# Performance work log

Measured on AMD Instinct MI355X. Metric: run time of the kernel, lower is better.

## Reference

```python
import jax, jax.numpy as jnp
import numpy as np

B, IN, H, OUT = 4096, 1024, 2048, 1024
EPS = 1e-5  # added to std (not variance), matching the torch module


def _ln(z, a, b):
    # torch.std default is unbiased (ddof=1); eps added to sigma
    mu = jnp.mean(z, axis=1, keepdims=True)
    sigma = jnp.std(z, axis=1, ddof=1, keepdims=True)
    return (z - mu) / (sigma + EPS) * a + b


def setup_inputs() -> dict:
    key = jax.random.key(0)
    ks = iter(jax.random.split(key, 40))
    W = lambda i, o: (jax.random.normal(next(ks), (o, i), jnp.float32) / np.sqrt(i)).astype(jnp.float32)
    bz = lambda o: jnp.zeros((o,), jnp.float32)
    d = {
        "inp": jax.random.normal(next(ks), (B, IN), jnp.float32),
        "h_0": jax.random.normal(next(ks), (B, H), jnp.float32),
        "c_0": jax.random.normal(next(ks), (B, H), jnp.float32),
        # h-side gate linears (H -> H)
        "Wfh": W(H, H), "bfh": bz(H), "Wih": W(H, H), "bih": bz(H),
        "Wch": W(H, H), "bch": bz(H), "Woh": W(H, H), "boh": bz(H),
        # x-side gate linears (IN -> H)
        "Wfx": W(IN, H), "bfx": bz(H), "Wix": W(IN, H), "bix": bz(H),
        "Wcx": W(IN, H), "bcx": bz(H), "Wox": W(IN, H), "box": bz(H),
        # decoder (H -> OUT)
        "Wdec": W(H, OUT), "bdec": bz(OUT),
        # LayerNormalization params (a2 ones, b2 zeros), shape (1, H)
        "ax": jnp.ones((1, H), jnp.float32), "bx": jnp.zeros((1, H), jnp.float32),
        "ah": jnp.ones((1, H), jnp.float32), "bh": jnp.zeros((1, H), jnp.float32),
        "ac": jnp.ones((1, H), jnp.float32), "bc": jnp.zeros((1, H), jnp.float32),
    }
    return d


def reference(inp, h_0, c_0,
              Wfh, bfh, Wih, bih, Wch, bch, Woh, boh,
              Wfx, bfx, Wix, bix, Wcx, bcx, Wox, box,
              Wdec, bdec, ax, bx, ah, bh, ac, bc):
    lin = lambda x, W, b: x @ W.T + b
    gate = lambda wx, bx_, wh, bh_: (_ln(lin(inp, wx, bx_), ax, bx)
                                     + _ln(lin(h_0, wh, bh_), ah, bh))
    f_g = jax.nn.sigmoid(gate(Wfx, bfx, Wfh, bfh))
    i_g = jax.nn.sigmoid(gate(Wix, bix, Wih, bih))
    c_tilda = jnp.tanh(gate(Wcx, bcx, Wch, bch))
    cx = f_g * c_0 + i_g * c_tilda
    o_g = jax.nn.sigmoid(gate(Wox, box, Woh, boh))
    hx = o_g * jnp.tanh(_ln(cx, ac, bc))
    out = lin(hx, Wdec, bdec)  # decoder applied to hidden state (vectorized over batch)
    return (out, hx, cx)
```

## Files before the change

kernel.cpp:

```cpp
#include <hip/hip_runtime.h>

#define NB   4096
#define NIN  1024
#define NH   2048
#define NOUT 1024
#define NH4  8192

typedef short short8 __attribute__((ext_vector_type(8)));
typedef float f32x4 __attribute__((ext_vector_type(4)));
typedef float f32x16 __attribute__((ext_vector_type(16)));
typedef unsigned short ushort8v __attribute__((ext_vector_type(8)));

__device__ __forceinline__ float bf2f(unsigned short u) {
  union { unsigned int i; float f; } c; c.i = ((unsigned int)u) << 16; return c.f;
}
__device__ __forceinline__ unsigned short f2bf(float f) {
  union { float f; unsigned int i; } c; c.f = f;
  unsigned int u = c.i;
  u += 0x7FFFu + ((u >> 16) & 1u);
  return (unsigned short)(u >> 16);
}
__device__ __forceinline__ float sigf(float x) { return 1.0f / (1.0f + __expf(-x)); }
__device__ __forceinline__ float tanh_f(float x) { return 1.0f - 2.0f / (__expf(2.0f * x) + 1.0f); }

#define CNT_INP  ((size_t)NB * NIN)
#define CNT_H0   ((size_t)NB * NH)
#define CNT_WXG  ((size_t)NH * NIN)
#define CNT_WHG  ((size_t)NH * NH)
#define CNT_WD   ((size_t)NOUT * NH)
#define OFF_XB   ((size_t)0)
#define OFF_H0B  (OFF_XB + CNT_INP)
#define OFF_HXB  (OFF_H0B + CNT_H0)
#define OFF_WX   (OFF_HXB + CNT_H0)
#define OFF_WH   (OFF_WX + 4 * CNT_WXG)
#define OFF_WD   (OFF_WH + 4 * CNT_WHG)
#define OFF_ZX   (OFF_WD + CNT_WD)
#define OFF_ZH   (OFF_ZX + (size_t)NB * NH4)
#define CVT_TOTAL (OFF_WD + CNT_WD)

struct CvtArgs { const float* src[11]; };

__global__ __launch_bounds__(256) void cvt_all(CvtArgs a, unsigned short* __restrict__ dstBase) {
  const size_t i = ((size_t)blockIdx.x * 256 + threadIdx.x) * 8;
  if (i >= CVT_TOTAL) return;
  const size_t cnt[11] = {CNT_INP, CNT_H0, CNT_WXG, CNT_WXG, CNT_WXG, CNT_WXG,
                          CNT_WHG, CNT_WHG, CNT_WHG, CNT_WHG, CNT_WD};
  const size_t dst[11] = {OFF_XB, OFF_H0B,
                          OFF_WX, OFF_WX + CNT_WXG, OFF_WX + 2 * CNT_WXG, OFF_WX + 3 * CNT_WXG,
                          OFF_WH, OFF_WH + CNT_WHG, OFF_WH + 2 * CNT_WHG, OFF_WH + 3 * CNT_WHG,
                          OFF_WD};
  size_t base = 0;
#pragma unroll
  for (int s = 0; s < 11; s++) {
    if (i < base + cnt[s]) {
      const size_t off = i - base;
      const float* sp = a.src[s] + off;
      float4 v0 = *(const float4*)(sp);
      float4 v1 = *(const float4*)(sp + 4);
      ushort8v o;
      o[0] = f2bf(v0.x); o[1] = f2bf(v0.y); o[2] = f2bf(v0.z); o[3] = f2bf(v0.w);
      o[4] = f2bf(v1.x); o[5] = f2bf(v1.y); o[6] = f2bf(v1.z); o[7] = f2bf(v1.w);
      *(ushort8v*)(dstBase + dst[s] + off) = o;
      return;
    }
    base += cnt[s];
  }
}

__device__ __forceinline__ void gload16(const void* g, void* l) {
  __builtin_amdgcn_global_load_lds((const __attribute__((address_space(1))) void*)g,
                                   (__attribute__((address_space(3))) void*)l, 16, 0, 0);
}

#define SCH0  __builtin_amdgcn_sched_barrier(0)
#define BARR  __builtin_amdgcn_s_barrier()
#define LGKM0 asm volatile("s_waitcnt lgkmcnt(0)" ::: "memory")
#define VMC6  asm volatile("s_waitcnt vmcnt(6)" ::: "memory")
#define VMC0  asm volatile("s_waitcnt vmcnt(0)" ::: "memory")
#define PRIO1 __builtin_amdgcn_s_setprio(1)
#define PRIO0 __builtin_amdgcn_s_setprio(0)
#define MFMA16(A, B, C) __builtin_amdgcn_mfma_f32_16x16x32_bf16((A), (B), (C), 0, 0, 0)

#define SWZ(R) (((R) & 7) ^ ((((R) >> 3) & 3) << 1))


__device__ __forceinline__ void stage_half(const unsigned short* __restrict__ G, size_t thrOff, int K,
                                           int R0, int H, int T, unsigned short* __restrict__ ldbase, int wid) {
  const unsigned short* gs = G + thrOff + (size_t)(R0 + H * 128) * K + (size_t)T * 64;
  unsigned short* ld = ldbase + (H * 128 + wid * 8) * 64;
  gload16(gs, ld);
  gload16(gs + (size_t)64 * K, ld + 4096);
}

__device__ __forceinline__ void tile_step(
    const unsigned short* __restrict__ sA, const unsigned short* __restrict__ sB,
    unsigned short* __restrict__ sAc, unsigned short* __restrict__ sBc, unsigned short* __restrict__ sAn,
    int t1, int t2,
    const unsigned short* __restrict__ Ag, const unsigned short* __restrict__ Bg,
    size_t thrOff, int m0, int n0, int K, int wid,
    const int (&oA)[8][2], const int (&oB)[4][2], f32x4 (&acc)[8][4]) {
  short8 b01[2][2], b23[2][2], alo[4][2], ahi[4][2];

#pragma unroll
  for (int n = 0; n < 2; n++) {
    b01[n][0] = *(const short8*)&sB[oB[n][0]];
    b01[n][1] = *(const short8*)&sB[oB[n][1]];
  }
#pragma unroll
  for (int m = 0; m < 2; m++) {
    alo[m][0] = *(const short8*)&sA[oA[m][0]];
    alo[m][1] = *(const short8*)&sA[oA[m][1]];
  }
  stage_half(Ag, thrOff, K, m0, 1, t1, sAn, wid);
  SCH0;
#pragma unroll
  for (int m = 2; m < 4; m++) {
    alo[m][0] = *(const short8*)&sA[oA[m][0]];
    alo[m][1] = *(const short8*)&sA[oA[m][1]];
  }
  SCH0;
  PRIO1;
#pragma unroll
  for (int m = 0; m < 2; m++)
#pragma unroll
    for (int n = 0; n < 2; n++) {
      acc[m][n] = MFMA16(alo[m][0], b01[n][0], acc[m][n]);
      acc[m][n] = MFMA16(alo[m][1], b01[n][1], acc[m][n]);
    }
  PRIO0; SCH0;
#pragma unroll
  for (int n = 0; n < 2; n++) {
    b23[n][0] = *(const short8*)&sB[oB[2 + n][0]];
    b23[n][1] = *(const short8*)&sB[oB[2 + n][1]];
  }
  SCH0;
  PRIO1;
#pragma unroll
  for (int m = 2; m < 4; m++)
#pragma unroll
    for (int n = 0; n < 2; n++) {
      acc[m][n] = MFMA16(alo[m][0], b01[n][0], acc[m][n]);
      acc[m][n] = MFMA16(alo[m][1], b01[n][1], acc[m][n]);
    }
  PRIO0; SCH0;
#pragma unroll
  for (int m = 0; m < 4; m++) {
    ahi[m][0] = *(const short8*)&sA[oA[4 + m][0]];
    ahi[m][1] = *(const short8*)&sA[oA[4 + m][1]];
  }
  SCH0;
  PRIO1;
#pragma unroll
  for (int m = 0; m < 4; m++)
#pragma unroll
    for (int n = 0; n < 2; n++) {
      acc[m][2 + n] = MFMA16(alo[m][0], b23[n][0], acc[m][2 + n]);
      acc[m][2 + n] = MFMA16(alo[m][1], b23[n][1], acc[m][2 + n]);
    }
  PRIO0;
  SCH0; BARR; SCH0;
  stage_half(Bg, thrOff, K, n0, 0, t2, sBc, wid);
  stage_half(Bg, thrOff, K, n0, 1, t2, sBc, wid);
  SCH0;
  PRIO1;
#pragma unroll
  for (int m = 0; m < 4; m++)
#pragma unroll
    for (int n = 0; n < 2; n++) {
      acc[4 + m][n] = MFMA16(ahi[m][0], b01[n][0], acc[4 + m][n]);
      acc[4 + m][n] = MFMA16(ahi[m][1], b01[n][1], acc[4 + m][n]);
    }
  PRIO0;
  SCH0; BARR; SCH0;
  stage_half(Ag, thrOff, K, m0, 0, t2, sAc, wid);
  SCH0;
  PRIO1;
#pragma unroll
  for (int m = 0; m < 4; m++)
#pragma unroll
    for (int n = 0; n < 2; n++) {
      acc[4 + m][2 + n] = MFMA16(ahi[m][0], b23[n][0], acc[4 + m][2 + n]);
      acc[4 + m][2 + n] = MFMA16(ahi[m][1], b23[n][1], acc[4 + m][2 + n]);
    }
  PRIO0;
  VMC6;
  SCH0; BARR; SCH0;
}

__global__ __launch_bounds__(512) void gemm_dual8(
    const unsigned short* __restrict__ Xb, const unsigned short* __restrict__ Wx,
    const unsigned short* __restrict__ H0b, const unsigned short* __restrict__ Wh,
    const float* bx0, const float* bx1, const float* bx2, const float* bx3,
    const float* bh0, const float* bh1, const float* bh2, const float* bh3,
    unsigned short* __restrict__ Zx, unsigned short* __restrict__ Zh) {
  __shared__ __align__(16) unsigned short As[2][256 * 64];
  __shared__ __align__(16) unsigned short Bs[2][256 * 64];

  const unsigned short* Ag; const unsigned short* Bg;
  const float *p0, *p1, *p2, *p3; unsigned short* Cg; int K;
  if (blockIdx.z == 0) { Ag = Xb;  Bg = Wx; Cg = Zx; K = NIN; p0 = bx0; p1 = bx1; p2 = bx2; p3 = bx3; }
  else                 { Ag = H0b; Bg = Wh; Cg = Zh; K = NH;  p0 = bh0; p1 = bh1; p2 = bh2; p3 = bh3; }

  const int t    = threadIdx.x;
  const int wid  = t >> 6;
  const int lane = t & 63;
  const int m15  = lane & 15;
  const int g4   = lane >> 4;
  const int wm   = wid >> 2;
  const int wn   = wid & 3;
  const int rloc = lane >> 3;
  const int slot = lane & 7;
  const int ck   = slot ^ rloc ^ ((wid & 3) << 1);
  const int m0   = blockIdx.y * 256;
  const int n0   = blockIdx.x * 256;
  const int NT   = K >> 6;
  const size_t thrOff = (size_t)(wid * 8 + rloc) * K + ck * 8;

  int oA[8][2], oB[4][2];
#pragma unroll
  for (int m = 0; m < 4; m++) {
    const int r1 = wm * 128 + m * 16 + m15;
    const int r2 = r1 + 64;
#pragma unroll
    for (int h = 0; h < 2; h++) {
      oA[m][h]     = r1 * 64 + (((h * 4 + g4) ^ SWZ(r1)) * 8);
      oA[4 + m][h] = r2 * 64 + (((h * 4 + g4) ^ SWZ(r2)) * 8);
    }
  }
#pragma unroll
  for (int n = 0; n < 4; n++) {
    const int r = wn * 64 + n * 16 + m15;
#pragma unroll
    for (int h = 0; h < 2; h++) oB[n][h] = r * 64 + (((h * 4 + g4) ^ SWZ(r)) * 8);
  }

  f32x4 acc[8][4];
#pragma unroll
  for (int m = 0; m < 8; m++)
#pragma unroll
    for (int n = 0; n < 4; n++)
#pragma unroll
      for (int r = 0; r < 4; r++) acc[m][n][r] = 0.f;

  stage_half(Ag, thrOff, K, m0, 0, 0, As[0], wid);
  stage_half(Ag, thrOff, K, m0, 1, 0, As[0], wid);
  stage_half(Bg, thrOff, K, n0, 0, 0, Bs[0], wid);
  stage_half(Bg, thrOff, K, n0, 1, 0, Bs[0], wid);
  stage_half(Bg, thrOff, K, n0, 0, 1, Bs[1], wid);
  stage_half(Bg, thrOff, K, n0, 1, 1, Bs[1], wid);
  stage_half(Ag, thrOff, K, m0, 0, 1, As[1], wid);
  VMC6;
  SCH0; BARR; SCH0;

  for (int kt = 0; kt < NT; kt += 2) {
    const int t2a = (kt + 2 < NT) ? kt + 2 : NT - 1;
    const int t1b = t2a;
    const int t2b = (kt + 3 < NT) ? kt + 3 : NT - 1;
    tile_step(As[0], Bs[0], As[0], Bs[0], As[1], kt + 1, t2a,
              Ag, Bg, thrOff, m0, n0, K, wid, oA, oB, acc);
    tile_step(As[1], Bs[1], As[1], Bs[1], As[0], t1b, t2b,
              Ag, Bg, thrOff, m0, n0, K, wid, oA, oB, acc);
  }

  VMC0;
  SCH0; BARR; SCH0;

  {
    unsigned short* wls = &As[0][0] + wid * (16 * 68);
    float bvn[4];
#pragma unroll
    for (int n = 0; n < 4; n++) {
      const int col = n0 + wn * 64 + n * 16 + m15;
      const float* bp = (col < 2048) ? p0 : ((col < 4096) ? p1 : ((col < 6144) ? p2 : p3));
      bvn[n] = bp[col & 2047];
    }
    const int lrow0 = lane >> 3;
    const int lcol0 = (lane & 7) * 8;
#pragma unroll
    for (int mt = 0; mt < 8; mt++) {
#pragma unroll
      for (int n = 0; n < 4; n++)
#pragma unroll
        for (int r = 0; r < 4; r++)
          wls[(g4 * 4 + r) * 68 + n * 16 + m15] = f2bf(acc[mt][n][r] + bvn[n]);
      LGKM0; SCH0;
#pragma unroll
      for (int i = 0; i < 2; i++) {
        const int lrow = i * 8 + lrow0;
        short8 v = *(const short8*)&wls[lrow * 68 + lcol0];
        *(short8*)&Cg[(size_t)(m0 + wm * 128 + mt * 16 + lrow) * NH4 + (n0 + wn * 64 + lcol0)] = v;
      }
      LGKM0; SCH0;
    }
  }
}

template<int MT, bool BOUT>
__device__ __forceinline__ void gemm_core32(const unsigned short* __restrict__ A,
                                            const unsigned short* __restrict__ Bm,
                                            const float* b0p, const float* b1p,
                                            const float* b2p, const float* b3p,
                                            float* __restrict__ Cf, unsigned short* __restrict__ Cb,
                                            int N, int K) {
  constexpr int TM = MT * 64;
  __shared__ __align__(16) unsigned short As[TM * 64];
  __shared__ __align__(16) unsigned short Bs[128 * 64];
  const int t = threadIdx.x;
  const int w = t >> 6;
  const int lane = t & 63;
  const int r31 = lane & 31;
  const int hi = lane >> 5;
  const int rloc = lane >> 3;
  const int slot = lane & 7;
  const int m0 = blockIdx.y * TM;
  const int n0 = blockIdx.x * 128;
  const int wm = (w >> 1) * (MT * 32);
  const int wn = (w & 1) * 64;

  f32x16 acc[MT][2];
#pragma unroll
  for (int i = 0; i < MT; i++)
#pragma unroll
    for (int j = 0; j < 2; j++)
#pragma unroll
      for (int r = 0; r < 16; r++) acc[i][j][r] = 0.f;

  const unsigned short* AgP[2 * MT];
  unsigned short* AsP[2 * MT];
#pragma unroll
  for (int q = 0; q < 2 * MT; q++) {
    const int iss = w + 4 * q;
    const int bblk = slot ^ rloc ^ (iss & 3);
    AgP[q] = A + (size_t)(m0 + iss * 8 + rloc) * K + bblk * 8;
    AsP[q] = As + iss * 512;
  }
  const unsigned short* BgP[4];
  unsigned short* BsP[4];
#pragma unroll
  for (int q = 0; q < 4; q++) {
    const int iss = w + 4 * q;
    const int bblk = slot ^ rloc ^ (iss & 3);
    BgP[q] = Bm + (size_t)(n0 + iss * 8 + rloc) * K + bblk * 8;
    BsP[q] = Bs + iss * 512;
  }

  const int swz = (r31 & 7) ^ ((r31 >> 3) & 3);

  for (int k0 = 0; k0 < K; k0 += 64) {
#pragma unroll
    for (int q = 0; q < 2 * MT; q++) gload16(AgP[q] + k0, AsP[q]);
#pragma unroll
    for (int q = 0; q < 4; q++) gload16(BgP[q] + k0, BsP[q]);
    __syncthreads();

#pragma unroll
    for (int ks = 0; ks < 4; ks++) {
      const int phys = ((ks * 2 + hi) ^ swz) * 8;
      short8 af[MT], bf[2];
#pragma unroll
      for (int mt = 0; mt < MT; mt++) af[mt] = *(const short8*)&As[(wm + mt * 32 + r31) * 64 + phys];
#pragma unroll
      for (int jt = 0; jt < 2; jt++) bf[jt] = *(const short8*)&Bs[(wn + jt * 32 + r31) * 64 + phys];
#pragma unroll
      for (int mt = 0; mt < MT; mt++)
#pragma unroll
        for (int jt = 0; jt < 2; jt++)
          acc[mt][jt] = __builtin_amdgcn_mfma_f32_32x32x16_bf16(af[mt], bf[jt], acc[mt][jt], 0, 0, 0);
    }
    __syncthreads();
  }

#pragma unroll
  for (int mt = 0; mt < MT; mt++) {
#pragma unroll
    for (int jt = 0; jt < 2; jt++) {
      const int col = n0 + wn + jt * 32 + r31;
      const float* bp = (col < 2048) ? b0p : ((col < 4096) ? b1p : ((col < 6144) ? b2p : b3p));
      const float bv = bp[col & 2047];
      const int rowb = m0 + wm + mt * 32 + hi * 4;
#pragma unroll
      for (int reg = 0; reg < 16; reg++) {
        const int row = rowb + (reg & 3) + 8 * (reg >> 2);
        const float v = acc[mt][jt][reg] + bv;
        const size_t idx = (size_t)row * N + col;
        if (BOUT) Cb[idx] = f2bf(v);
        else      Cf[idx] = v;
      }
    }
  }
}

__global__ __launch_bounds__(256) void gemm_dec(const unsigned short* __restrict__ HXb,
                                                const unsigned short* __restrict__ Wd,
                                                const float* __restrict__ bdec,
                                                float* __restrict__ out) {
  gemm_core32<1, false>(HXb, Wd, bdec, bdec, bdec, bdec, out, nullptr, NOUT, NH);
}

__global__ __launch_bounds__(256) void ln_gates(const unsigned short* __restrict__ Zx,
                                                const unsigned short* __restrict__ Zh,
                                                const float* __restrict__ c0,
                                                const float* __restrict__ ax, const float* __restrict__ bx,
                                                const float* __restrict__ ah, const float* __restrict__ bh,
                                                const float* __restrict__ ac, const float* __restrict__ bc,
                                                float* __restrict__ out_top,
                                                unsigned short* __restrict__ hx_bf) {
  const int b = blockIdx.x;
  const int t = threadIdx.x;
  const int n = t * 8;
  const int w = t >> 6;
  const int lane = t & 63;
  const float inv_n = 1.0f / 2048.0f, inv_nm1 = 1.0f / 2047.0f;

  short8 zx[4], zh[4];
  const size_t rowoff = (size_t)b * NH4;
#pragma unroll
  for (int g = 0; g < 4; g++) {
    zx[g] = *(const short8*)(Zx + rowoff + g * NH + n);
    zh[g] = *(const short8*)(Zh + rowoff + g * NH + n);
  }

  float s[16];
#pragma unroll
  for (int g = 0; g < 4; g++) {
    float su = 0, sq = 0, su2 = 0, sq2 = 0;
#pragma unroll
    for (int j = 0; j < 8; j++) {
      float v = bf2f((unsigned short)zx[g][j]); su += v; sq += v * v;
      float u = bf2f((unsigned short)zh[g][j]); su2 += u; sq2 += u * u;
    }
    s[g * 4 + 0] = su; s[g * 4 + 1] = sq; s[g * 4 + 2] = su2; s[g * 4 + 3] = sq2;
  }
#pragma unroll
  for (int i = 0; i < 16; i++) {
    float v = s[i];
#pragma unroll
    for (int o = 32; o > 0; o >>= 1) v += __shfl_xor(v, o, 64);
    s[i] = v;
  }
  __shared__ float red[4][16];
  __shared__ float red2[4][2];
  if (lane == 0) {
#pragma unroll
    for (int i = 0; i < 16; i++) red[w][i] = s[i];
  }
  __syncthreads();
#pragma unroll
  for (int i = 0; i < 16; i++) s[i] = red[0][i] + red[1][i] + red[2][i] + red[3][i];

  float mux[4], ivx[4], muh[4], ivh[4];
#pragma unroll
  for (int g = 0; g < 4; g++) {
    mux[g] = s[g * 4 + 0] * inv_n;
    float vx = fmaxf((s[g * 4 + 1] - s[g * 4 + 0] * mux[g]) * inv_nm1, 0.0f);
    ivx[g] = 1.0f / (sqrtf(vx) + 1e-5f);
    muh[g] = s[g * 4 + 2] * inv_n;
    float vh = fmaxf((s[g * 4 + 3] - s[g * 4 + 2] * muh[g]) * inv_nm1, 0.0f);
    ivh[g] = 1.0f / (sqrtf(vh) + 1e-5f);
  }

  float axl[8], bxl[8], ahl[8], bhl[8], c0l[8];
  *(float4*)&axl[0] = *(const float4*)(ax + n); *(float4*)&axl[4] = *(const float4*)(ax + n + 4);
  *(float4*)&bxl[0] = *(const float4*)(bx + n); *(float4*)&bxl[4] = *(const float4*)(bx + n + 4);
  *(float4*)&ahl[0] = *(const float4*)(ah + n); *(float4*)&ahl[4] = *(const float4*)(ah + n + 4);
  *(float4*)&bhl[0] = *(const float4*)(bh + n); *(float4*)&bhl[4] = *(const float4*)(bh + n + 4);
  const float* c0p = c0 + (size_t)b * NH + n;
  *(float4*)&c0l[0] = *(const float4*)(c0p); *(float4*)&c0l[4] = *(const float4*)(c0p + 4);

  float cx[8], og[8];
  float cs = 0, css = 0;
#pragma unroll
  for (int j = 0; j < 8; j++) {
    float pre[4];
#pragma unroll
    for (int g = 0; g < 4; g++) {
      float vx = bf2f((unsigned short)zx[g][j]);
      float vh = bf2f((unsigned short)zh[g][j]);
      pre[g] = ((vx - mux[g]) * ivx[g]) * axl[j] + bxl[j]
             + ((vh - muh[g]) * ivh[g]) * ahl[j] + bhl[j];
    }
    float fg = sigf(pre[0]);
    float ig = sigf(pre[1]);
    float ct = tanh_f(pre[2]);
    og[j] = sigf(pre[3]);
    float c = fg * c0l[j] + ig * ct;
    cx[j] = c; cs += c; css += c * c;
  }
#pragma unroll
  for (int o = 32; o > 0; o >>= 1) { cs += __shfl_xor(cs, o, 64); css += __shfl_xor(css, o, 64); }
  if (lane == 0) { red2[w][0] = cs; red2[w][1] = css; }
  __syncthreads();
  cs = red2[0][0] + red2[1][0] + red2[2][0] + red2[3][0];
  css = red2[0][1] + red2[1][1] + red2[2][1] + red2[3][1];
  const float muc = cs * inv_n;
  const float varc = fmaxf((css - cs * muc) * inv_nm1, 0.0f);
  const float ivc = 1.0f / (sqrtf(varc) + 1e-5f);

  float acl[8], bcl[8];
  *(float4*)&acl[0] = *(const float4*)(ac + n); *(float4*)&acl[4] = *(const float4*)(ac + n + 4);
  *(float4*)&bcl[0] = *(const float4*)(bc + n); *(float4*)&bcl[4] = *(const float4*)(bc + n + 4);

  float hx[8];
#pragma unroll
  for (int j = 0; j < 8; j++)
    hx[j] = og[j] * tanh_f((cx[j] - muc) * ivc * acl[j] + bcl[j]);

  float* hx_out = out_top + (size_t)NB * NOUT + (size_t)b * NH + n;
  float* cx_out = out_top + (size_t)NB * NOUT + (size_t)NB * NH + (size_t)b * NH + n;
  float4 v;
  v.x = hx[0]; v.y = hx[1]; v.z = hx[2]; v.w = hx[3]; *(float4*)(hx_out) = v;
  v.x = hx[4]; v.y = hx[5]; v.z = hx[6]; v.w = hx[7]; *(float4*)(hx_out + 4) = v;
  v.x = cx[0]; v.y = cx[1]; v.z = cx[2]; v.w = cx[3]; *(float4*)(cx_out) = v;
  v.x = cx[4]; v.y = cx[5]; v.z = cx[6]; v.w = cx[7]; *(float4*)(cx_out + 4) = v;
  ushort8v hb;
#pragma unroll
  for (int j = 0; j < 8; j++) hb[j] = f2bf(hx[j]);
  *(ushort8v*)(hx_bf + (size_t)b * NH + n) = hb;
}

extern "C" void kernel_launch(void* const* d_in, const int* in_sizes, int n_in,
                              void* d_out, int out_size, void* d_ws, size_t ws_size,
                              hipStream_t stream) {
  const float* inp = (const float*)d_in[0];
  const float* h0  = (const float*)d_in[1];
  const float* c0  = (const float*)d_in[2];
  const float* bhg[4] = {(const float*)d_in[4], (const float*)d_in[6], (const float*)d_in[8], (const float*)d_in[10]};
  const float* bxg[4] = {(const float*)d_in[12], (const float*)d_in[14], (const float*)d_in[16], (const float*)d_in[18]};
  const float* bdec = (const float*)d_in[20];
  const float* ax = (const float*)d_in[21];
  const float* bx = (const float*)d_in[22];
  const float* ah = (const float*)d_in[23];
  const float* bh = (const float*)d_in[24];
  const float* ac = (const float*)d_in[25];
  const float* bc = (const float*)d_in[26];

  unsigned short* wsb = (unsigned short*)d_ws;
  unsigned short* Xb   = wsb + OFF_XB;
  unsigned short* H0b  = wsb + OFF_H0B;
  unsigned short* HXb  = wsb + OFF_HXB;
  unsigned short* Wx4b = wsb + OFF_WX;
  unsigned short* Wh4b = wsb + OFF_WH;
  unsigned short* Wdb  = wsb + OFF_WD;
  unsigned short* Zx   = wsb + OFF_ZX;
  unsigned short* Zh   = wsb + OFF_ZH;

  CvtArgs ca;
  ca.src[0] = inp; ca.src[1] = h0;
  ca.src[2] = (const float*)d_in[11]; ca.src[3] = (const float*)d_in[13];
  ca.src[4] = (const float*)d_in[15]; ca.src[5] = (const float*)d_in[17];
  ca.src[6] = (const float*)d_in[3];  ca.src[7] = (const float*)d_in[5];
  ca.src[8] = (const float*)d_in[7];  ca.src[9] = (const float*)d_in[9];
  ca.src[10] = (const float*)d_in[19];
  {
    const size_t nthr = CVT_TOTAL / 8;
    cvt_all<<<dim3((unsigned)((nthr + 255) / 256)), dim3(256), 0, stream>>>(ca, wsb);
  }

  gemm_dual8<<<dim3(NH4 / 256, NB / 256, 2), 512, 0, stream>>>(
      Xb, Wx4b, H0b, Wh4b,
      bxg[0], bxg[1], bxg[2], bxg[3],
      bhg[0], bhg[1], bhg[2], bhg[3],
      Zx, Zh);

  ln_gates<<<dim3(NB), 256, 0, stream>>>(Zx, Zh, c0, ax, bx, ah, bh, ac, bc, (float*)d_out, HXb);

  gemm_dec<<<dim3(NOUT / 128, NB / 64), 256, 0, stream>>>(HXb, Wdb, bdec, (float*)d_out);
}
```

Before: 561.5 us.

## Switch dual gate GEMM to 32x32x16 bf16 MFMA tiles

Replaces the 16x16x32 MFMA inner loop of the dual gate GEMM with 32x32x16 MFMA instructions. Each wave now holds 4x2 32x32 accumulator tiles instead of 8x4 16x16 tiles, and the LDS fragment offsets, load schedule and epilogue write-back are remapped to the 32x32 output register layout. The aim is fewer LDS fragment reads per FLOP and fewer MFMA issues. In exchange the interleaving of global staging and barriers with compute is reordered, and the last MFMA group now runs after the barrier, which could change how well loads overlap with math.

```diff
diff --git a/kernel.cpp b/kernel.cpp
--- a/kernel.cpp
+++ b/kernel.cpp
@@ -79,7 +79,7 @@
 #define VMC0  asm volatile("s_waitcnt vmcnt(0)" ::: "memory")
 #define PRIO1 __builtin_amdgcn_s_setprio(1)
 #define PRIO0 __builtin_amdgcn_s_setprio(0)
-#define MFMA16(A, B, C) __builtin_amdgcn_mfma_f32_16x16x32_bf16((A), (B), (C), 0, 0, 0)
+#define MFMA32(A, B, C) __builtin_amdgcn_mfma_f32_32x32x16_bf16((A), (B), (C), 0, 0, 0)
 
 #define SWZ(R) (((R) & 7) ^ ((((R) >> 3) & 3) << 1))
 
@@ -92,99 +92,66 @@
   gload16(gs + (size_t)64 * K, ld + 4096);
 }
 
-__device__ __forceinline__ void tile_step(
+__device__ __forceinline__ void tile_step32(
     const unsigned short* __restrict__ sA, const unsigned short* __restrict__ sB,
-    unsigned short* __restrict__ sAc, unsigned short* __restrict__ sBc, unsigned short* __restrict__ sAn,
+    unsigned short* __restrict__ sAn,
+    unsigned short* __restrict__ sAc, unsigned short* __restrict__ sBc,
     int t1, int t2,
     const unsigned short* __restrict__ Ag, const unsigned short* __restrict__ Bg,
     size_t thrOff, int m0, int n0, int K, int wid,
-    const int (&oA)[8][2], const int (&oB)[4][2], f32x4 (&acc)[8][4]) {
-  short8 b01[2][2], b23[2][2], alo[4][2], ahi[4][2];
-
-#pragma unroll
-  for (int n = 0; n < 2; n++) {
-    b01[n][0] = *(const short8*)&sB[oB[n][0]];
-    b01[n][1] = *(const short8*)&sB[oB[n][1]];
-  }
-#pragma unroll
-  for (int m = 0; m < 2; m++) {
-    alo[m][0] = *(const short8*)&sA[oA[m][0]];
-    alo[m][1] = *(const short8*)&sA[oA[m][1]];
-  }
+    const int (&oA)[4][4], const int (&oB)[2][4], f32x16 (&acc)[4][2]) {
+  short8 a[4][4], b[2][4];
+
+#pragma unroll
+  for (int ks = 0; ks < 4; ks++) b[0][ks] = *(const short8*)&sB[oB[0][ks]];
+#pragma unroll
+  for (int mt = 0; mt < 2; mt++)
+#pragma unroll
+    for (int ks = 0; ks < 4; ks++) a[mt][ks] = *(const short8*)&sA[oA[mt][ks]];
   stage_half(Ag, thrOff, K, m0, 1, t1, sAn, wid);
   SCH0;
 #pragma unroll
-  for (int m = 2; m < 4; m++) {
-    alo[m][0] = *(const short8*)&sA[oA[m][0]];
-    alo[m][1] = *(const short8*)&sA[oA[m][1]];
-  }
+  for (int ks = 0; ks < 4; ks++) b[1][ks] = *(const short8*)&sB[oB[1][ks]];
+  SCH0;
+#pragma unroll
+  for (int mt = 2; mt < 4; mt++)
+#pragma unroll
+    for (int ks = 0; ks < 4; ks++) a[mt][ks] = *(const short8*)&sA[oA[mt][ks]];
   SCH0;
   PRIO1;
 #pragma unroll
-  for (int m = 0; m < 2; m++)
-#pragma unroll
-    for (int n = 0; n < 2; n++) {
-      acc[m][n] = MFMA16(alo[m][0], b01[n][0], acc[m][n]);
-      acc[m][n] = MFMA16(alo[m][1], b01[n][1], acc[m][n]);
-    }
+  for (int ks = 0; ks < 4; ks++)
+#pragma unroll
+    for (int mt = 0; mt < 2; mt++)
+      acc[mt][0] = MFMA32(a[mt][ks], b[0][ks], acc[mt][0]);
   PRIO0; SCH0;
-#pragma unroll
-  for (int n = 0; n < 2; n++) {
-    b23[n][0] = *(const short8*)&sB[oB[2 + n][0]];
-    b23[n][1] = *(const short8*)&sB[oB[2 + n][1]];
-  }
-  SCH0;
   PRIO1;
 #pragma unroll
-  for (int m = 2; m < 4; m++)
-#pragma unroll
-    for (int n = 0; n < 2; n++) {
-      acc[m][n] = MFMA16(alo[m][0], b01[n][0], acc[m][n]);
-      acc[m][n] = MFMA16(alo[m][1], b01[n][1], acc[m][n]);
-    }
+  for (int ks = 0; ks < 4; ks++)
+#pragma unroll
+    for (int mt = 0; mt < 2; mt++)
+      acc[mt][1] = MFMA32(a[mt][ks], b[1][ks], acc[mt][1]);
   PRIO0; SCH0;
-#pragma unroll
-  for (int m = 0; m < 4; m++) {
-    ahi[m][0] = *(const short8*)&sA[oA[4 + m][0]];
-    ahi[m][1] = *(const short8*)&sA[oA[4 + m][1]];
-  }
-  SCH0;
   PRIO1;
 #pragma unroll
-  for (int m = 0; m < 4; m++)
-#pragma unroll
-    for (int n = 0; n < 2; n++) {
-      acc[m][2 + n] = MFMA16(alo[m][0], b23[n][0], acc[m][2 + n]);
-      acc[m][2 + n] = MFMA16(alo[m][1], b23[n][1], acc[m][2 + n]);
-    }
+  for (int ks = 0; ks < 4; ks++)
+#pragma unroll
+    for (int mt = 2; mt < 4; mt++)
+      acc[mt][0] = MFMA32(a[mt][ks], b[0][ks], acc[mt][0]);
   PRIO0;
   SCH0; BARR; SCH0;
   stage_half(Bg, thrOff, K, n0, 0, t2, sBc, wid);
   stage_half(Bg, thrOff, K, n0, 1, t2, sBc, wid);
-  SCH0;
-  PRIO1;
-#pragma unroll
-  for (int m = 0; m < 4; m++)
-#pragma unroll
-    for (int n = 0; n < 2; n++) {
-      acc[4 + m][n] = MFMA16(ahi[m][0], b01[n][0], acc[4 + m][n]);
-      acc[4 + m][n] = MFMA16(ahi[m][1], b01[n][1], acc[4 + m][n]);
-    }
-  PRIO0;
-  SCH0; BARR; SCH0;
   stage_half(Ag, thrOff, K, m0, 0, t2, sAc, wid);
-  SCH0;
-  PRIO1;
-#pragma unroll
-  for (int m = 0; m < 4; m++)
-#pragma unroll
-    for (int n = 0; n < 2; n++) {
-      acc[4 + m][2 + n] = MFMA16(ahi[m][0], b23[n][0], acc[4 + m][2 + n]);
-      acc[4 + m][2 + n] = MFMA16(ahi[m][1], b23[n][1], acc[4 + m][2 + n]);
-    }
-  PRIO0;
   VMC6;
   SCH0; BARR; SCH0;
+  PRIO1;
+#pragma unroll
+  for (int ks = 0; ks < 4; ks++)
+#pragma unroll
+    for (int mt = 2; mt < 4; mt++)
+      acc[mt][1] = MFMA32(a[mt][ks], b[1][ks], acc[mt][1]);
+  PRIO0; SCH0;
 }
 
 __global__ __launch_bounds__(512) void gemm_dual8(
@@ -204,8 +171,8 @@
   const int t    = threadIdx.x;
   const int wid  = t >> 6;
   const int lane = t & 63;
-  const int m15  = lane & 15;
-  const int g4   = lane >> 4;
+  const int r31  = lane & 31;
+  const int hi   = lane >> 5;
   const int wm   = wid >> 2;
   const int wn   = wid & 3;
   const int rloc = lane >> 3;
@@ -216,31 +183,27 @@
   const int NT   = K >> 6;
   const size_t thrOff = (size_t)(wid * 8 + rloc) * K + ck * 8;
 
-  int oA[8][2], oB[4][2];
-#pragma unroll
-  for (int m = 0; m < 4; m++) {
-    const int r1 = wm * 128 + m * 16 + m15;
-    const int r2 = r1 + 64;
-#pragma unroll
-    for (int h = 0; h < 2; h++) {
-      oA[m][h]     = r1 * 64 + (((h * 4 + g4) ^ SWZ(r1)) * 8);
-      oA[4 + m][h] = r2 * 64 + (((h * 4 + g4) ^ SWZ(r2)) * 8);
-    }
-  }
-#pragma unroll
-  for (int n = 0; n < 4; n++) {
-    const int r = wn * 64 + n * 16 + m15;
-#pragma unroll
-    for (int h = 0; h < 2; h++) oB[n][h] = r * 64 + (((h * 4 + g4) ^ SWZ(r)) * 8);
-  }
-
-  f32x4 acc[8][4];
-#pragma unroll
-  for (int m = 0; m < 8; m++)
-#pragma unroll
-    for (int n = 0; n < 4; n++)
-#pragma unroll
-      for (int r = 0; r < 4; r++) acc[m][n][r] = 0.f;
+  int oA[4][4], oB[2][4];
+#pragma unroll
+  for (int mt = 0; mt < 4; mt++) {
+    const int row = wm * 128 + mt * 32 + r31;
+#pragma unroll
+    for (int ks = 0; ks < 4; ks++) oA[mt][ks] = row * 64 + (((ks * 2 + hi) ^ SWZ(row)) * 8);
+  }
+#pragma unroll
+  for (int jt = 0; jt < 2; jt++) {
+    const int row = wn * 64 + jt * 32 + r31;
+#pragma unroll
+    for (int ks = 0; ks < 4; ks++) oB[jt][ks] = row * 64 + (((ks * 2 + hi) ^ SWZ(row)) * 8);
+  }
+
+  f32x16 acc[4][2];
+#pragma unroll
+  for (int m = 0; m < 4; m++)
+#pragma unroll
+    for (int n = 0; n < 2; n++)
+#pragma unroll
+      for (int r = 0; r < 16; r++) acc[m][n][r] = 0.f;
 
   stage_half(Ag, thrOff, K, m0, 0, 0, As[0], wid);
   stage_half(Ag, thrOff, K, m0, 1, 0, As[0], wid);
@@ -254,41 +217,42 @@
 
   for (int kt = 0; kt < NT; kt += 2) {
     const int t2a = (kt + 2 < NT) ? kt + 2 : NT - 1;
-    const int t1b = t2a;
     const int t2b = (kt + 3 < NT) ? kt + 3 : NT - 1;
-    tile_step(As[0], Bs[0], As[0], Bs[0], As[1], kt + 1, t2a,
-              Ag, Bg, thrOff, m0, n0, K, wid, oA, oB, acc);
-    tile_step(As[1], Bs[1], As[1], Bs[1], As[0], t1b, t2b,
-              Ag, Bg, thrOff, m0, n0, K, wid, oA, oB, acc);
+    tile_step32(As[0], Bs[0], As[1], As[0], Bs[0], kt + 1, t2a,
+                Ag, Bg, thrOff, m0, n0, K, wid, oA, oB, acc);
+    tile_step32(As[1], Bs[1], As[0], As[1], Bs[1], t2a, t2b,
+                Ag, Bg, thrOff, m0, n0, K, wid, oA, oB, acc);
   }
 
   VMC0;
   SCH0; BARR; SCH0;
 
   {
-    unsigned short* wls = &As[0][0] + wid * (16 * 68);
-    float bvn[4];
-#pragma unroll
-    for (int n = 0; n < 4; n++) {
-      const int col = n0 + wn * 64 + n * 16 + m15;
+    unsigned short* wls = &As[0][0] + wid * (32 * 68);
+    float bvn[2];
+#pragma unroll
+    for (int jt = 0; jt < 2; jt++) {
+      const int col = n0 + wn * 64 + jt * 32 + r31;
       const float* bp = (col < 2048) ? p0 : ((col < 4096) ? p1 : ((col < 6144) ? p2 : p3));
-      bvn[n] = bp[col & 2047];
+      bvn[jt] = bp[col & 2047];
     }
     const int lrow0 = lane >> 3;
     const int lcol0 = (lane & 7) * 8;
 #pragma unroll
-    for (int mt = 0; mt < 8; mt++) {
-#pragma unroll
-      for (int n = 0; n < 4; n++)
-#pragma unroll
-        for (int r = 0; r < 4; r++)
-          wls[(g4 * 4 + r) * 68 + n * 16 + m15] = f2bf(acc[mt][n][r] + bvn[n]);
+    for (int mt = 0; mt < 4; mt++) {
+#pragma unroll
+      for (int jt = 0; jt < 2; jt++)
+#pragma unroll
+        for (int reg = 0; reg < 16; reg++) {
+          const int lr = hi * 4 + (reg & 3) + 8 * (reg >> 2);
+          wls[lr * 68 + jt * 32 + r31] = f2bf(acc[mt][jt][reg] + bvn[jt]);
+        }
       LGKM0; SCH0;
 #pragma unroll
-      for (int i = 0; i < 2; i++) {
+      for (int i = 0; i < 4; i++) {
         const int lrow = i * 8 + lrow0;
         short8 v = *(const short8*)&wls[lrow * 68 + lcol0];
-        *(short8*)&Cg[(size_t)(m0 + wm * 128 + mt * 16 + lrow) * NH4 + (n0 + wn * 64 + lcol0)] = v;
+        *(short8*)&Cg[(size_t)(m0 + wm * 128 + mt * 32 + lrow) * NH4 + (n0 + wn * 64 + lcol0)] = v;
       }
       LGKM0; SCH0;
     }
```

Result: slower. 573.2 us (+2.1%).
